# Optimization experiments

Hardware: AMD Instinct MI355X
Metric: run time of the kernel (lower is better)

## Reference

```python
import jax, jax.numpy as jnp
import numpy as np

D = 768
NH = 8
HD = D // NH
DFF = 2048
EPS = 1e-5


def _layer_norm(x, g, b):
    mu = jnp.mean(x, axis=-1, keepdims=True)
    var = jnp.mean(jnp.square(x - mu), axis=-1, keepdims=True)
    return (x - mu) * jax.lax.rsqrt(var + EPS) * g + b


def setup_inputs() -> dict:
    key = jax.random.key(0)
    ks = jax.random.split(key, 16)
    B, L = 2, 2048
    s = 0.02
    return {
        "x": jax.random.normal(ks[0], (B, L, D), jnp.float32),
        "attn_bias": jax.random.normal(ks[1], (B, L, L), jnp.float32),
        "in_proj_w": jax.random.normal(ks[2], (3 * D, D), jnp.float32) * s,
        "in_proj_b": jnp.zeros((3 * D,), jnp.float32),
        "out_w": jax.random.normal(ks[3], (D, D), jnp.float32) * s,
        "out_b": jnp.zeros((D,), jnp.float32),
        "W1": jax.random.normal(ks[4], (DFF, D), jnp.float32) * s,
        "b1": jnp.zeros((DFF,), jnp.float32),
        "W2": jax.random.normal(ks[5], (D, DFF), jnp.float32) * s,
        "b2": jnp.zeros((D,), jnp.float32),
        "g1": jnp.ones((D,), jnp.float32),
        "be1": jnp.zeros((D,), jnp.float32),
        "g2": jnp.ones((D,), jnp.float32),
        "be2": jnp.zeros((D,), jnp.float32),
    }


def reference(x, attn_bias, in_proj_w, in_proj_b, out_w, out_b,
              W1, b1, W2, b2, g1, be1, g2, be2):
    B, L, _ = x.shape
    # fused qkv projection (torch nn.MultiheadAttention in_proj)
    qkv = x @ in_proj_w.T + in_proj_b          # [B, L, 3D]
    q, k, v = jnp.split(qkv, 3, axis=-1)
    q = q.reshape(B, L, NH, HD).transpose(0, 2, 1, 3)  # [B, nH, L, hd]
    k = k.reshape(B, L, NH, HD).transpose(0, 2, 1, 3)
    v = v.reshape(B, L, NH, HD).transpose(0, 2, 1, 3)
    scale = 1.0 / jnp.sqrt(jnp.asarray(HD, x.dtype))
    scores = jnp.einsum("bhqd,bhkd->bhqk", q * scale, k)
    scores = scores + attn_bias[:, None, :, :]         # broadcast over heads == expand
    attn = jax.nn.softmax(scores, axis=-1)
    ctx = jnp.einsum("bhqk,bhkd->bhqd", attn, v)       # [B, nH, L, hd]
    ctx = ctx.transpose(0, 2, 1, 3).reshape(B, L, D)
    attn_out = ctx @ out_w.T + out_b
    x = _layer_norm(x + attn_out, g1, be1)
    h = jax.nn.gelu(x @ W1.T + b1, approximate=False)  # torch default GELU = erf
    ff = h @ W2.T + b2
    return _layer_norm(x + ff, g2, be2)
```

## Files before the change

### kernel.cpp

```cpp
#include <hip/hip_runtime.h>
#include <hip/hip_bf16.h>
#include <math.h>

typedef __bf16 bf16;
typedef __attribute__((ext_vector_type(8))) __bf16 bf16x8;
typedef __attribute__((ext_vector_type(4))) __bf16 bf16x4;
typedef __attribute__((ext_vector_type(4))) float f32x4;

#define LOG2E 1.4426950408889634f

__device__ __forceinline__ void gload16(const bf16* g, bf16* l) {
  __builtin_amdgcn_global_load_lds(
      (const __attribute__((address_space(1))) void*)g,
      (__attribute__((address_space(3))) void*)l, 16, 0, 0);
}

struct CastSegs { const float* src[5]; bf16* dst[5]; };

__global__ void fused_cast_kernel(CastSegs segs) {
  const int e0 = 786432, e1 = 1228800, e2 = 1376256, e3 = 1769472, e4 = 2162688;
  int i = blockIdx.x * blockDim.x + threadIdx.x;
  int stride = gridDim.x * blockDim.x;
  for (; i < e4; i += stride) {
    int s = 0, base = 0;
    if (i >= e0) { s = 1; base = e0; }
    if (i >= e1) { s = 2; base = e1; }
    if (i >= e2) { s = 3; base = e2; }
    if (i >= e3) { s = 4; base = e3; }
    float4 v = ((const float4*)segs.src[s])[i - base];
    bf16x4 o = { (bf16)v.x, (bf16)v.y, (bf16)v.z, (bf16)v.w };
    ((bf16x4*)segs.dst[s])[i - base] = o;
  }
}

template<int MODE>
__launch_bounds__(256)
__global__ void gemm_kernel(const bf16* __restrict__ A, const bf16* __restrict__ W,
                            const float* __restrict__ bias, bf16* __restrict__ vt,
                            void* __restrict__ out, int K, int O) {
  __shared__ bf16 As[128 * 64];
  __shared__ bf16 Bs[128 * 64];
  const int t    = threadIdx.x;
  const int lane = t & 63;
  const int wave = t >> 6;
  const int wr = (wave >> 1) * 64;
  const int wc = (wave & 1) * 64;
  const int n0 = blockIdx.y * 128;
  const int o0 = blockIdx.x * 128;

  f32x4 zero = {0.f, 0.f, 0.f, 0.f};
  f32x4 acc[4][4];
#pragma unroll
  for (int m = 0; m < 4; m++)
#pragma unroll
    for (int n = 0; n < 4; n++) acc[m][n] = zero;

  const int fr  = lane & 15;
  const int fg8 = (lane >> 4) * 8;

  for (int k0 = 0; k0 < K; k0 += 64) {
    __syncthreads();
#pragma unroll
    for (int c = 0; c < 4; c++) {
      int f = c * 256 + t;
      int row = f >> 3;
      int col = (f & 7) * 8;
      gload16(&A[(size_t)(n0 + row) * K + k0 + col], &As[f * 8]);
      gload16(&W[(size_t)(o0 + row) * K + k0 + col], &Bs[f * 8]);
    }
    __syncthreads();
#pragma unroll
    for (int kf = 0; kf < 2; kf++) {
      bf16x8 a[4], b[4];
#pragma unroll
      for (int m = 0; m < 4; m++) a[m] = *(const bf16x8*)&As[(wr + m * 16 + fr) * 64 + kf * 32 + fg8];
#pragma unroll
      for (int n = 0; n < 4; n++) b[n] = *(const bf16x8*)&Bs[(wc + n * 16 + fr) * 64 + kf * 32 + fg8];
#pragma unroll
      for (int m = 0; m < 4; m++)
#pragma unroll
        for (int n = 0; n < 4; n++)
          acc[m][n] = __builtin_amdgcn_mfma_f32_16x16x32_bf16(a[m], b[n], acc[m][n], 0, 0, 0);
    }
  }

  const int fg4 = (lane >> 4) * 4;
#pragma unroll
  for (int m = 0; m < 4; m++) {
#pragma unroll
    for (int n = 0; n < 4; n++) {
      int col = o0 + wc + n * 16 + fr;
      float bv = bias[col];
      if constexpr (MODE == 3) {
        if (col >= 1536) {
          int c = col - 1536;
          int h = c / 96;
          int hd = c - h * 96;
          int row0 = n0 + wr + m * 16 + fg4;
          int b = row0 >> 11;
          int token = row0 & 2047;
          bf16x4 ov;
#pragma unroll
          for (int r = 0; r < 4; r++) ov[r] = (bf16)(acc[m][n][r] + bv);
          *(bf16x4*)&vt[((size_t)((b * 8 + h) * 96 + hd)) * 2048 + token] = ov;
          continue;
        }
      }
#pragma unroll
      for (int r = 0; r < 4; r++) {
        int row = n0 + wr + m * 16 + fg4 + r;
        float v = acc[m][n][r] + bv;
        if constexpr (MODE == 2) {
          v = 0.5f * v * (1.0f + erff(v * 0.70710678118654752f));
          ((bf16*)out)[(size_t)row * O + col] = (bf16)v;
        } else {
          ((bf16*)out)[(size_t)row * O + col] = (bf16)v;
        }
      }
    }
  }
}

__launch_bounds__(256)
__global__ void gemmW_kernel(const bf16* __restrict__ A, const bf16* __restrict__ W,
                             const float* __restrict__ bias, const float* __restrict__ res,
                             float* __restrict__ out, int K, int O) {
  __shared__ bf16 As[128 * 64];
  __shared__ bf16 Bs[64 * 64];
  const int t    = threadIdx.x;
  const int lane = t & 63;
  const int wave = t >> 6;
  const int wr = wave * 32;
  const int n0 = blockIdx.y * 128;
  const int o0 = blockIdx.x * 64;

  f32x4 zero = {0.f, 0.f, 0.f, 0.f};
  f32x4 acc[2][4];
#pragma unroll
  for (int m = 0; m < 2; m++)
#pragma unroll
    for (int n = 0; n < 4; n++) acc[m][n] = zero;

  const int fr  = lane & 15;
  const int fg8 = (lane >> 4) * 8;

  for (int k0 = 0; k0 < K; k0 += 64) {
    __syncthreads();
#pragma unroll
    for (int c = 0; c < 4; c++) {
      int f = c * 256 + t;
      int row = f >> 3;
      int col = (f & 7) * 8;
      gload16(&A[(size_t)(n0 + row) * K + k0 + col], &As[f * 8]);
    }
#pragma unroll
    for (int c = 0; c < 2; c++) {
      int f = c * 256 + t;
      int row = f >> 3;
      int col = (f & 7) * 8;
      gload16(&W[(size_t)(o0 + row) * K + k0 + col], &Bs[f * 8]);
    }
    __syncthreads();
#pragma unroll
    for (int kf = 0; kf < 2; kf++) {
      bf16x8 a[2], b[4];
#pragma unroll
      for (int m = 0; m < 2; m++) a[m] = *(const bf16x8*)&As[(wr + m * 16 + fr) * 64 + kf * 32 + fg8];
#pragma unroll
      for (int n = 0; n < 4; n++) b[n] = *(const bf16x8*)&Bs[(n * 16 + fr) * 64 + kf * 32 + fg8];
#pragma unroll
      for (int m = 0; m < 2; m++)
#pragma unroll
        for (int n = 0; n < 4; n++)
          acc[m][n] = __builtin_amdgcn_mfma_f32_16x16x32_bf16(a[m], b[n], acc[m][n], 0, 0, 0);
    }
  }

  const int fg4 = (lane >> 4) * 4;
#pragma unroll
  for (int m = 0; m < 2; m++) {
#pragma unroll
    for (int n = 0; n < 4; n++) {
      int col = o0 + n * 16 + fr;
      float bv = bias[col];
#pragma unroll
      for (int r = 0; r < 4; r++) {
        int row = n0 + wr + m * 16 + fg4 + r;
        float v = acc[m][n][r] + bv + res[(size_t)row * O + col];
        out[(size_t)row * O + col] = v;
      }
    }
  }
}

__launch_bounds__(512, 4)
__global__ void attn_kernel(const bf16* __restrict__ qkv, const bf16* __restrict__ vt,
                            const float* __restrict__ bias, float* __restrict__ opart,
                            float* __restrict__ ml) {
  __shared__ bf16 Ks[2][64][104];
  __shared__ bf16 Vs[2][96][72];
  __shared__ bf16 Pl[8][16][72];
  const int t    = threadIdx.x;
  const int lane = t & 63;
  const int wave = t >> 6;
  const int qb = blockIdx.x, h = blockIdx.y;
  const int half = blockIdx.z & 1, b = blockIdx.z >> 1;
  const int kvstart = half * 1024;
  const int q0 = qb * 128 + wave * 16;
  const int fq = lane & 15;
  const int g  = lane >> 4;
  const size_t base = (size_t)b * 2048 * 2304;

  bf16x8 qf[3];
  {
    const bf16* qp = qkv + base + (size_t)(q0 + fq) * 2304 + h * 96;
#pragma unroll
    for (int f = 0; f < 3; f++) qf[f] = *(const bf16x8*)(qp + f * 32 + g * 8);
  }

  const int kr1 = t >> 3, kc1 = (t & 7) * 8;
  const int kr2 = t >> 2, kc2 = 64 + (t & 3) * 8;
  const int vr2 = 64 + (t >> 3);
  const bf16* kbase = qkv + base + (size_t)kvstart * 2304 + 768 + h * 96;
  const bf16* vbase = vt + (size_t)((b * 8 + h) * 96) * 2048 + kvstart;

  bf16x8 kreg0, kreg1, vreg0, vreg1;
  const bool lo = (t < 256);

  kreg0 = *(const bf16x8*)(kbase + (size_t)kr1 * 2304 + kc1);
  vreg0 = *(const bf16x8*)(vbase + (size_t)kr1 * 2048 + kc1);
  if (lo) {
    kreg1 = *(const bf16x8*)(kbase + (size_t)kr2 * 2304 + kc2);
    vreg1 = *(const bf16x8*)(vbase + (size_t)vr2 * 2048 + kc1);
  }

  float m_run = -1e30f, l_run = 0.f;
  f32x4 zero = {0.f, 0.f, 0.f, 0.f};
  f32x4 o_acc[6];
#pragma unroll
  for (int i = 0; i < 6; i++) o_acc[i] = zero;

  const float scale = 0.10206207261596575f;
  const float* bp = bias + ((size_t)b * 2048 + q0 + fq) * 2048 + kvstart;

  int cur = 0;
  for (int kv0 = 0; kv0 < 1024; kv0 += 64) {
    *(bf16x8*)&Ks[cur][kr1][kc1] = kreg0;
    *(bf16x8*)&Vs[cur][kr1][kc1] = vreg0;
    if (lo) {
      *(bf16x8*)&Ks[cur][kr2][kc2] = kreg1;
      *(bf16x8*)&Vs[cur][vr2][kc1] = vreg1;
    }
    __syncthreads();

    if (kv0 + 64 < 1024) {
      int nx = kv0 + 64;
      kreg0 = *(const bf16x8*)(kbase + (size_t)(nx + kr1) * 2304 + kc1);
      vreg0 = *(const bf16x8*)(vbase + (size_t)kr1 * 2048 + nx + kc1);
      if (lo) {
        kreg1 = *(const bf16x8*)(kbase + (size_t)(nx + kr2) * 2304 + kc2);
        vreg1 = *(const bf16x8*)(vbase + (size_t)vr2 * 2048 + nx + kc1);
      }
    }
    __builtin_amdgcn_sched_barrier(0);

    float4 bf[4];
#pragma unroll
    for (int kvt = 0; kvt < 4; kvt++)
      bf[kvt] = *(const float4*)(bp + kv0 + kvt * 16 + g * 4);

    f32x4 s[4];
#pragma unroll
    for (int kvt = 0; kvt < 4; kvt++) {
      s[kvt] = zero;
#pragma unroll
      for (int f = 0; f < 3; f++) {
        bf16x8 kfr = *(const bf16x8*)&Ks[cur][kvt * 16 + fq][f * 32 + g * 8];
        s[kvt] = __builtin_amdgcn_mfma_f32_16x16x32_bf16(kfr, qf[f], s[kvt], 0, 0, 0);
      }
    }

    float p[4][4];
    float vmax = -1e30f;
#pragma unroll
    for (int kvt = 0; kvt < 4; kvt++) {
#pragma unroll
      for (int r = 0; r < 4; r++) {
        float sv = fmaf(s[kvt][r], scale, (&bf[kvt].x)[r]);
        p[kvt][r] = sv;
        vmax = fmaxf(vmax, sv);
      }
    }
    vmax = fmaxf(vmax, __shfl_xor(vmax, 16));
    vmax = fmaxf(vmax, __shfl_xor(vmax, 32));
    if (!__all(vmax <= m_run + 8.0f)) {
      float m_new = fmaxf(m_run, vmax);
      float corr = exp2f((m_run - m_new) * LOG2E);
      l_run *= corr;
#pragma unroll
      for (int i = 0; i < 6; i++)
#pragma unroll
        for (int r = 0; r < 4; r++) o_acc[i][r] *= corr;
      m_run = m_new;
    }
    float rsum = 0.f;
#pragma unroll
    for (int kvt = 0; kvt < 4; kvt++) {
      bf16x4 pb;
#pragma unroll
      for (int r = 0; r < 4; r++) {
        float pv = exp2f((p[kvt][r] - m_run) * LOG2E);
        rsum += pv;
        pb[r] = (bf16)pv;
      }
      *(bf16x4*)&Pl[wave][fq][kvt * 16 + g * 4] = pb;
    }
    rsum += __shfl_xor(rsum, 16);
    rsum += __shfl_xor(rsum, 32);
    l_run += rsum;

#pragma unroll
    for (int kf = 0; kf < 2; kf++) {
      bf16x8 pfrag = *(const bf16x8*)&Pl[wave][fq][kf * 32 + g * 8];
#pragma unroll
      for (int ht = 0; ht < 6; ht++) {
        bf16x8 vfrag = *(const bf16x8*)&Vs[cur][ht * 16 + fq][kf * 32 + g * 8];
        o_acc[ht] = __builtin_amdgcn_mfma_f32_16x16x32_bf16(vfrag, pfrag, o_acc[ht], 0, 0, 0);
      }
    }
    cur ^= 1;
  }

  float* op = opart + (size_t)half * (16 * 2048 * 96) + ((size_t)(b * 8 + h) * 2048 + q0 + fq) * 96;
  float* mlp = ml + ((size_t)half * 32768 + (size_t)(b * 8 + h) * 2048 + q0 + fq) * 2;
#pragma unroll
  for (int ht = 0; ht < 6; ht++)
    *(f32x4*)&op[ht * 16 + g * 4] = o_acc[ht];
  if (g == 0) { mlp[0] = m_run; mlp[1] = l_run; }
}

__launch_bounds__(256)
__global__ void attn_combine_kernel(const float* __restrict__ opart, const float* __restrict__ ml,
                                    bf16* __restrict__ ctx) {
  int idx = blockIdx.x * blockDim.x + threadIdx.x;
  if (idx >= 786432) return;
  int e = idx * 4;
  int bh = e / (2048 * 96);
  int rem = e - bh * (2048 * 96);
  int q = rem / 96;
  int hd = rem - q * 96;
  const float* op0 = opart;
  const float* op1 = opart + (size_t)16 * 2048 * 96;
  float4 o1 = *(const float4*)&op0[e];
  float4 o2 = *(const float4*)&op1[e];
  const float* ml0 = ml + (size_t)(bh * 2048 + q) * 2;
  const float* ml1 = ml0 + (size_t)32768 * 2;
  float m1 = ml0[0], l1 = ml0[1];
  float m2 = ml1[0], l2 = ml1[1];
  float M = fmaxf(m1, m2);
  float w1 = exp2f((m1 - M) * LOG2E);
  float w2 = exp2f((m2 - M) * LOG2E);
  float inv = 1.0f / (l1 * w1 + l2 * w2);
  int b = bh >> 3, h = bh & 7;
  bf16x4 o;
  o[0] = (bf16)((o1.x * w1 + o2.x * w2) * inv);
  o[1] = (bf16)((o1.y * w1 + o2.y * w2) * inv);
  o[2] = (bf16)((o1.z * w1 + o2.z * w2) * inv);
  o[3] = (bf16)((o1.w * w1 + o2.w * w2) * inv);
  *(bf16x4*)&ctx[((size_t)b * 2048 + q) * 768 + h * 96 + hd] = o;
}

__launch_bounds__(256)
__global__ void ln_kernel(const float* in, const float* __restrict__ gamma,
                          const float* __restrict__ beta, float* outf, bf16* outb) {
  const int row = blockIdx.x;
  const int t = threadIdx.x;
  const float* rp = in + (size_t)row * 768;
  float v[3];
#pragma unroll
  for (int i = 0; i < 3; i++) v[i] = rp[t + 256 * i];
  float s = v[0] + v[1] + v[2];
  float ss = v[0] * v[0] + v[1] * v[1] + v[2] * v[2];
#pragma unroll
  for (int off = 1; off < 64; off <<= 1) {
    s += __shfl_xor(s, off);
    ss += __shfl_xor(ss, off);
  }
  __shared__ float red[8];
  if ((t & 63) == 0) { red[(t >> 6) * 2] = s; red[(t >> 6) * 2 + 1] = ss; }
  __syncthreads();
  s = red[0] + red[2] + red[4] + red[6];
  ss = red[1] + red[3] + red[5] + red[7];
  float mu = s * (1.0f / 768.0f);
  float var = ss * (1.0f / 768.0f) - mu * mu;
  float rs = rsqrtf(var + 1e-5f);
#pragma unroll
  for (int i = 0; i < 3; i++) {
    int col = t + 256 * i;
    float y = (v[i] - mu) * rs * gamma[col] + beta[col];
    outf[(size_t)row * 768 + col] = y;
    if (outb) outb[(size_t)row * 768 + col] = (bf16)y;
  }
}

extern "C" void kernel_launch(void* const* d_in, const int* in_sizes, int n_in,
                              void* d_out, int out_size, void* d_ws, size_t ws_size,
                              hipStream_t stream) {
  (void)in_sizes; (void)n_in; (void)out_size; (void)ws_size;
  const float* x     = (const float*)d_in[0];
  const float* ab    = (const float*)d_in[1];
  const float* w_qkv = (const float*)d_in[2];
  const float* b_qkv = (const float*)d_in[3];
  const float* w_out = (const float*)d_in[4];
  const float* b_out = (const float*)d_in[5];
  const float* W1    = (const float*)d_in[6];
  const float* b1    = (const float*)d_in[7];
  const float* W2    = (const float*)d_in[8];
  const float* b2    = (const float*)d_in[9];
  const float* g1    = (const float*)d_in[10];
  const float* be1   = (const float*)d_in[11];
  const float* g2    = (const float*)d_in[12];
  const float* be2   = (const float*)d_in[13];
  float* outf = (float*)d_out;

  char* p = (char*)d_ws;
  bf16* xb    = (bf16*)p;  p += (size_t)4096 * 768 * 2;
  bf16* qkv   = (bf16*)p;  p += (size_t)4096 * 2304 * 2;
  bf16* ctx   = (bf16*)p;  p += (size_t)4096 * 768 * 2;
  float* x1f  = (float*)p; p += (size_t)4096 * 768 * 4;
  bf16* x1b   = (bf16*)p;  p += (size_t)4096 * 768 * 2;
  bf16* hbuf  = (bf16*)p;  p += (size_t)4096 * 2048 * 2;
  bf16* wqkvb = (bf16*)p;  p += (size_t)2304 * 768 * 2;
  bf16* woutb = (bf16*)p;  p += (size_t)768 * 768 * 2;
  bf16* w1b   = (bf16*)p;  p += (size_t)2048 * 768 * 2;
  bf16* w2b   = (bf16*)p;  p += (size_t)768 * 2048 * 2;
  float* opart = (float*)p; p += (size_t)2 * 16 * 2048 * 96 * 4;
  float* mlb   = (float*)p; p += (size_t)2 * 32768 * 2 * 4;
  bf16* vtb   = (bf16*)x1f;

  CastSegs segs;
  segs.src[0] = x;     segs.dst[0] = xb;
  segs.src[1] = w_qkv; segs.dst[1] = wqkvb;
  segs.src[2] = w_out; segs.dst[2] = woutb;
  segs.src[3] = W1;    segs.dst[3] = w1b;
  segs.src[4] = W2;    segs.dst[4] = w2b;
  fused_cast_kernel<<<2048, 256, 0, stream>>>(segs);

  gemm_kernel<3><<<dim3(18, 32), 256, 0, stream>>>(xb, wqkvb, b_qkv, vtb, qkv, 768, 2304);
  attn_kernel<<<dim3(16, 8, 4), 512, 0, stream>>>(qkv, vtb, ab, opart, mlb);
  attn_combine_kernel<<<3072, 256, 0, stream>>>(opart, mlb, ctx);
  gemmW_kernel<<<dim3(12, 32), 256, 0, stream>>>(ctx, woutb, b_out, x, outf, 768, 768);
  ln_kernel<<<4096, 256, 0, stream>>>(outf, g1, be1, x1f, x1b);
  gemm_kernel<2><<<dim3(16, 32), 256, 0, stream>>>(x1b, w1b, b1, nullptr, hbuf, 768, 2048);
  gemmW_kernel<<<dim3(12, 32), 256, 0, stream>>>(hbuf, w2b, b2, x1f, outf, 2048, 768);
  ln_kernel<<<4096, 256, 0, stream>>>(outf, g2, be2, outf, nullptr);
}
```

Measured before the change: 216.5 us.

## Give each attention wave two query sub-tiles and shuffle P in registers

The attention kernel now uses 256 threads, with each wave handling 32 query rows as two 16-row sub-tiles. Each K and V fragment read from LDS now feeds two MFMAs instead of one. The probability matrix is rearranged into the MFMA operand layout with cross-lane shuffles rather than a round trip through shared memory, and the K/V shared buffers are single-buffered with two barriers per iteration. This cuts LDS traffic and LDS footprint but raises register pressure, halves threads per block, and drops the double buffering.

```diff
diff --git a/kernel.cpp b/kernel.cpp
--- a/kernel.cpp
+++ b/kernel.cpp
@@ -5,6 +5,7 @@
 typedef __bf16 bf16;
 typedef __attribute__((ext_vector_type(8))) __bf16 bf16x8;
 typedef __attribute__((ext_vector_type(4))) __bf16 bf16x4;
+typedef __attribute__((ext_vector_type(2))) __bf16 bf16x2;
 typedef __attribute__((ext_vector_type(4))) float f32x4;
 
 #define LOG2E 1.4426950408889634f
@@ -13,6 +14,11 @@
   __builtin_amdgcn_global_load_lds(
       (const __attribute__((address_space(1))) void*)g,
       (__attribute__((address_space(3))) void*)l, 16, 0, 0);
+}
+
+__device__ __forceinline__ unsigned packbf2(float a, float b) {
+  bf16x2 v = { (bf16)a, (bf16)b };
+  return __builtin_bit_cast(unsigned, v);
 }
 
 struct CastSegs { const float* src[5]; bf16* dst[5]; };
@@ -193,150 +199,188 @@
   }
 }
 
-__launch_bounds__(512, 4)
+__launch_bounds__(256, 2)
 __global__ void attn_kernel(const bf16* __restrict__ qkv, const bf16* __restrict__ vt,
                             const float* __restrict__ bias, float* __restrict__ opart,
                             float* __restrict__ ml) {
-  __shared__ bf16 Ks[2][64][104];
-  __shared__ bf16 Vs[2][96][72];
-  __shared__ bf16 Pl[8][16][72];
+  __shared__ bf16 Ks[64 * 104];
+  __shared__ bf16 Vs[96 * 72];
   const int t    = threadIdx.x;
   const int lane = t & 63;
   const int wave = t >> 6;
   const int qb = blockIdx.x, h = blockIdx.y;
   const int half = blockIdx.z & 1, b = blockIdx.z >> 1;
   const int kvstart = half * 1024;
-  const int q0 = qb * 128 + wave * 16;
+  const int q0 = qb * 128 + wave * 32;
   const int fq = lane & 15;
   const int g  = lane >> 4;
   const size_t base = (size_t)b * 2048 * 2304;
 
-  bf16x8 qf[3];
-  {
-    const bf16* qp = qkv + base + (size_t)(q0 + fq) * 2304 + h * 96;
-#pragma unroll
-    for (int f = 0; f < 3; f++) qf[f] = *(const bf16x8*)(qp + f * 32 + g * 8);
-  }
-
-  const int kr1 = t >> 3, kc1 = (t & 7) * 8;
-  const int kr2 = t >> 2, kc2 = 64 + (t & 3) * 8;
-  const int vr2 = 64 + (t >> 3);
+  bf16x8 qf[2][3];
+#pragma unroll
+  for (int ss = 0; ss < 2; ss++) {
+    const bf16* qp = qkv + base + (size_t)(q0 + ss * 16 + fq) * 2304 + h * 96;
+#pragma unroll
+    for (int f = 0; f < 3; f++) qf[ss][f] = *(const bf16x8*)(qp + f * 32 + g * 8);
+  }
+
+  const int krow = t >> 2, kcb = (t & 3) * 24;
   const bf16* kbase = qkv + base + (size_t)kvstart * 2304 + 768 + h * 96;
   const bf16* vbase = vt + (size_t)((b * 8 + h) * 96) * 2048 + kvstart;
 
-  bf16x8 kreg0, kreg1, vreg0, vreg1;
-  const bool lo = (t < 256);
-
-  kreg0 = *(const bf16x8*)(kbase + (size_t)kr1 * 2304 + kc1);
-  vreg0 = *(const bf16x8*)(vbase + (size_t)kr1 * 2048 + kc1);
-  if (lo) {
-    kreg1 = *(const bf16x8*)(kbase + (size_t)kr2 * 2304 + kc2);
-    vreg1 = *(const bf16x8*)(vbase + (size_t)vr2 * 2048 + kc1);
-  }
-
-  float m_run = -1e30f, l_run = 0.f;
+  bf16x8 kreg[3], vreg[3];
+#pragma unroll
+  for (int i = 0; i < 3; i++) {
+    kreg[i] = *(const bf16x8*)(kbase + (size_t)krow * 2304 + kcb + i * 8);
+    int c = t + 256 * i;
+    vreg[i] = *(const bf16x8*)(vbase + (size_t)(c >> 3) * 2048 + (c & 7) * 8);
+  }
+
+  float m_run[2] = {-1e30f, -1e30f}, l_run[2] = {0.f, 0.f};
   f32x4 zero = {0.f, 0.f, 0.f, 0.f};
-  f32x4 o_acc[6];
-#pragma unroll
-  for (int i = 0; i < 6; i++) o_acc[i] = zero;
+  f32x4 o_acc[2][6];
+#pragma unroll
+  for (int ss = 0; ss < 2; ss++)
+#pragma unroll
+    for (int i = 0; i < 6; i++) o_acc[ss][i] = zero;
 
   const float scale = 0.10206207261596575f;
-  const float* bp = bias + ((size_t)b * 2048 + q0 + fq) * 2048 + kvstart;
-
-  int cur = 0;
+  const float* bp[2];
+  bp[0] = bias + ((size_t)b * 2048 + q0 + fq) * 2048 + kvstart;
+  bp[1] = bp[0] + (size_t)16 * 2048;
+
+  bf16x8 pb[2][2];
+
   for (int kv0 = 0; kv0 < 1024; kv0 += 64) {
-    *(bf16x8*)&Ks[cur][kr1][kc1] = kreg0;
-    *(bf16x8*)&Vs[cur][kr1][kc1] = vreg0;
-    if (lo) {
-      *(bf16x8*)&Ks[cur][kr2][kc2] = kreg1;
-      *(bf16x8*)&Vs[cur][vr2][kc1] = vreg1;
-    }
-    __syncthreads();
-
+    if (kv0) __syncthreads();
+    *(bf16x8*)&Ks[krow * 104 + kcb]      = kreg[0];
+    *(bf16x8*)&Ks[krow * 104 + kcb + 8]  = kreg[1];
+    *(bf16x8*)&Ks[krow * 104 + kcb + 16] = kreg[2];
+#pragma unroll
+    for (int i = 0; i < 3; i++) {
+      int c = t + 256 * i;
+      *(bf16x8*)&Vs[(c >> 3) * 72 + (c & 7) * 8] = vreg[i];
+    }
     if (kv0 + 64 < 1024) {
       int nx = kv0 + 64;
-      kreg0 = *(const bf16x8*)(kbase + (size_t)(nx + kr1) * 2304 + kc1);
-      vreg0 = *(const bf16x8*)(vbase + (size_t)kr1 * 2048 + nx + kc1);
-      if (lo) {
-        kreg1 = *(const bf16x8*)(kbase + (size_t)(nx + kr2) * 2304 + kc2);
-        vreg1 = *(const bf16x8*)(vbase + (size_t)vr2 * 2048 + nx + kc1);
+#pragma unroll
+      for (int i = 0; i < 3; i++) {
+        kreg[i] = *(const bf16x8*)(kbase + (size_t)(nx + krow) * 2304 + kcb + i * 8);
+        int c = t + 256 * i;
+        vreg[i] = *(const bf16x8*)(vbase + (size_t)(c >> 3) * 2048 + nx + (c & 7) * 8);
       }
     }
     __builtin_amdgcn_sched_barrier(0);
-
-    float4 bf[4];
-#pragma unroll
-    for (int kvt = 0; kvt < 4; kvt++)
-      bf[kvt] = *(const float4*)(bp + kv0 + kvt * 16 + g * 4);
-
-    f32x4 s[4];
+    __syncthreads();
+
+    float4 bf[2][4];
+#pragma unroll
+    for (int ss = 0; ss < 2; ss++)
+#pragma unroll
+      for (int kvt = 0; kvt < 4; kvt++)
+        bf[ss][kvt] = *(const float4*)(bp[ss] + kv0 + kvt * 16 + g * 4);
+
+    f32x4 s[2][4];
 #pragma unroll
     for (int kvt = 0; kvt < 4; kvt++) {
-      s[kvt] = zero;
+      s[0][kvt] = zero;
+      s[1][kvt] = zero;
 #pragma unroll
       for (int f = 0; f < 3; f++) {
-        bf16x8 kfr = *(const bf16x8*)&Ks[cur][kvt * 16 + fq][f * 32 + g * 8];
-        s[kvt] = __builtin_amdgcn_mfma_f32_16x16x32_bf16(kfr, qf[f], s[kvt], 0, 0, 0);
-      }
-    }
-
-    float p[4][4];
-    float vmax = -1e30f;
-#pragma unroll
-    for (int kvt = 0; kvt < 4; kvt++) {
-#pragma unroll
-      for (int r = 0; r < 4; r++) {
-        float sv = fmaf(s[kvt][r], scale, (&bf[kvt].x)[r]);
-        p[kvt][r] = sv;
-        vmax = fmaxf(vmax, sv);
-      }
-    }
-    vmax = fmaxf(vmax, __shfl_xor(vmax, 16));
-    vmax = fmaxf(vmax, __shfl_xor(vmax, 32));
-    if (!__all(vmax <= m_run + 8.0f)) {
-      float m_new = fmaxf(m_run, vmax);
-      float corr = exp2f((m_run - m_new) * LOG2E);
-      l_run *= corr;
-#pragma unroll
-      for (int i = 0; i < 6; i++)
-#pragma unroll
-        for (int r = 0; r < 4; r++) o_acc[i][r] *= corr;
-      m_run = m_new;
-    }
-    float rsum = 0.f;
-#pragma unroll
-    for (int kvt = 0; kvt < 4; kvt++) {
-      bf16x4 pb;
-#pragma unroll
-      for (int r = 0; r < 4; r++) {
-        float pv = exp2f((p[kvt][r] - m_run) * LOG2E);
-        rsum += pv;
-        pb[r] = (bf16)pv;
-      }
-      *(bf16x4*)&Pl[wave][fq][kvt * 16 + g * 4] = pb;
-    }
-    rsum += __shfl_xor(rsum, 16);
-    rsum += __shfl_xor(rsum, 32);
-    l_run += rsum;
+        bf16x8 kfr = *(const bf16x8*)&Ks[(kvt * 16 + fq) * 104 + f * 32 + g * 8];
+        s[0][kvt] = __builtin_amdgcn_mfma_f32_16x16x32_bf16(kfr, qf[0][f], s[0][kvt], 0, 0, 0);
+        s[1][kvt] = __builtin_amdgcn_mfma_f32_16x16x32_bf16(kfr, qf[1][f], s[1][kvt], 0, 0, 0);
+      }
+    }
+
+#pragma unroll
+    for (int ss = 0; ss < 2; ss++) {
+      float p[4][4];
+      float vmax = -1e30f;
+#pragma unroll
+      for (int kvt = 0; kvt < 4; kvt++)
+#pragma unroll
+        for (int r = 0; r < 4; r++) {
+          float sv = fmaf(s[ss][kvt][r], scale, (&bf[ss][kvt].x)[r]);
+          p[kvt][r] = sv;
+          vmax = fmaxf(vmax, sv);
+        }
+      vmax = fmaxf(vmax, __shfl_xor(vmax, 16));
+      vmax = fmaxf(vmax, __shfl_xor(vmax, 32));
+      if (!__all(vmax <= m_run[ss] + 8.0f)) {
+        float m_new = fmaxf(m_run[ss], vmax);
+        float corr = exp2f((m_run[ss] - m_new) * LOG2E);
+        l_run[ss] *= corr;
+#pragma unroll
+        for (int i = 0; i < 6; i++)
+#pragma unroll
+          for (int r = 0; r < 4; r++) o_acc[ss][i][r] *= corr;
+        m_run[ss] = m_new;
+      }
+      float rsum = 0.f;
+      uint2 d[4];
+#pragma unroll
+      for (int kvt = 0; kvt < 4; kvt++) {
+        float e0 = exp2f((p[kvt][0] - m_run[ss]) * LOG2E);
+        float e1 = exp2f((p[kvt][1] - m_run[ss]) * LOG2E);
+        float e2 = exp2f((p[kvt][2] - m_run[ss]) * LOG2E);
+        float e3 = exp2f((p[kvt][3] - m_run[ss]) * LOG2E);
+        rsum += (e0 + e1) + (e2 + e3);
+        d[kvt].x = packbf2(e0, e1);
+        d[kvt].y = packbf2(e2, e3);
+      }
+      rsum += __shfl_xor(rsum, 16);
+      rsum += __shfl_xor(rsum, 32);
+      l_run[ss] += rsum;
+
+      bool glow = (g < 2);
+      uint2 snd0 = glow ? d[1] : d[0];
+      uint2 snd1 = glow ? d[3] : d[2];
+      uint2 r0, r1;
+      r0.x = __shfl_xor(snd0.x, 32); r0.y = __shfl_xor(snd0.y, 32);
+      r1.x = __shfl_xor(snd1.x, 32); r1.y = __shfl_xor(snd1.y, 32);
+      uint2 k0 = glow ? d[0] : d[1];
+      uint2 k1 = glow ? d[2] : d[3];
+      bool sendk = ((g ^ (g >> 1)) & 1);
+      uint2 s0 = sendk ? k0 : r0;
+      uint2 s1 = sendk ? k1 : r1;
+      uint2 q0_, q1_;
+      q0_.x = __shfl_xor(s0.x, 16); q0_.y = __shfl_xor(s0.y, 16);
+      q1_.x = __shfl_xor(s1.x, 16); q1_.y = __shfl_xor(s1.y, 16);
+      uint2 kept0 = sendk ? r0 : k0;
+      uint2 kept1 = sendk ? r1 : k1;
+      bool godd = (g & 1);
+      uint2 lo0 = godd ? q0_ : kept0;
+      uint2 hi0 = godd ? kept0 : q0_;
+      uint2 lo1 = godd ? q1_ : kept1;
+      uint2 hi1 = godd ? kept1 : q1_;
+      uint4 u0 = { lo0.x, lo0.y, hi0.x, hi0.y };
+      uint4 u1 = { lo1.x, lo1.y, hi1.x, hi1.y };
+      pb[ss][0] = __builtin_bit_cast(bf16x8, u0);
+      pb[ss][1] = __builtin_bit_cast(bf16x8, u1);
+    }
 
 #pragma unroll
     for (int kf = 0; kf < 2; kf++) {
-      bf16x8 pfrag = *(const bf16x8*)&Pl[wave][fq][kf * 32 + g * 8];
 #pragma unroll
       for (int ht = 0; ht < 6; ht++) {
-        bf16x8 vfrag = *(const bf16x8*)&Vs[cur][ht * 16 + fq][kf * 32 + g * 8];
-        o_acc[ht] = __builtin_amdgcn_mfma_f32_16x16x32_bf16(vfrag, pfrag, o_acc[ht], 0, 0, 0);
-      }
-    }
-    cur ^= 1;
-  }
-
-  float* op = opart + (size_t)half * (16 * 2048 * 96) + ((size_t)(b * 8 + h) * 2048 + q0 + fq) * 96;
-  float* mlp = ml + ((size_t)half * 32768 + (size_t)(b * 8 + h) * 2048 + q0 + fq) * 2;
-#pragma unroll
-  for (int ht = 0; ht < 6; ht++)
-    *(f32x4*)&op[ht * 16 + g * 4] = o_acc[ht];
-  if (g == 0) { mlp[0] = m_run; mlp[1] = l_run; }
+        bf16x8 vfr = *(const bf16x8*)&Vs[(ht * 16 + fq) * 72 + kf * 32 + g * 8];
+        o_acc[0][ht] = __builtin_amdgcn_mfma_f32_16x16x32_bf16(vfr, pb[0][kf], o_acc[0][ht], 0, 0, 0);
+        o_acc[1][ht] = __builtin_amdgcn_mfma_f32_16x16x32_bf16(vfr, pb[1][kf], o_acc[1][ht], 0, 0, 0);
+      }
+    }
+  }
+
+#pragma unroll
+  for (int ss = 0; ss < 2; ss++) {
+    int q = q0 + ss * 16 + fq;
+    float* op = opart + (size_t)half * (16 * 2048 * 96) + ((size_t)(b * 8 + h) * 2048 + q) * 96;
+    float* mlp = ml + ((size_t)half * 32768 + (size_t)(b * 8 + h) * 2048 + q) * 2;
+#pragma unroll
+    for (int ht = 0; ht < 6; ht++)
+      *(f32x4*)&op[ht * 16 + g * 4] = o_acc[ss][ht];
+    if (g == 0) { mlp[0] = m_run[ss]; mlp[1] = l_run[ss]; }
+  }
 }
 
 __launch_bounds__(256)
@@ -447,7 +491,7 @@
   fused_cast_kernel<<<2048, 256, 0, stream>>>(segs);
 
   gemm_kernel<3><<<dim3(18, 32), 256, 0, stream>>>(xb, wqkvb, b_qkv, vtb, qkv, 768, 2304);
-  attn_kernel<<<dim3(16, 8, 4), 512, 0, stream>>>(qkv, vtb, ab, opart, mlb);
+  attn_kernel<<<dim3(16, 8, 4), 256, 0, stream>>>(qkv, vtb, ab, opart, mlb);
   attn_combine_kernel<<<3072, 256, 0, stream>>>(opart, mlb, ctx);
   gemmW_kernel<<<dim3(12, 32), 256, 0, stream>>>(ctx, woutb, b_out, x, outf, 768, 768);
   ln_kernel<<<4096, 256, 0, stream>>>(outf, g1, be1, x1f, x1b);
```

Result: no change. 219.9 us (+1.6%).
